# Kernel tuning notes

Measured on AMD Instinct MI355X. Metric: run time of the kernel, lower is better.

## Reference

```python
import jax, jax.numpy as jnp
import numpy as np

THRESHOLD = 0.9
N = 20000
K = 32
F = 64


def setup_inputs() -> dict:
    key = jax.random.key(0)
    k1, k2, k3, k4, k5 = jax.random.split(key, 5)
    features = jax.random.normal(k1, (N, F), dtype=jnp.float32)
    score = jax.random.normal(k2, (N, 1), dtype=jnp.float32)
    distances = jax.random.uniform(k3, (N, K), dtype=jnp.float32)
    # two equal segments; neighbours sampled within own segment, self at col 0
    row_splits = jnp.array([0, N // 2, N], dtype=jnp.int32)
    segN = N // 2
    local_self = (jnp.arange(N, dtype=jnp.int32) % segN)
    seg_start = (jnp.arange(N, dtype=jnp.int32) // segN) * segN
    r = jax.random.randint(k4, (N, K - 1), 0, segN - 1, dtype=jnp.int32)
    r = r + (r >= local_self[:, None]).astype(jnp.int32)  # avoid sampling self
    neigh = seg_start[:, None] + r
    nidxs = jnp.concatenate([jnp.arange(N, dtype=jnp.int32)[:, None], neigh], axis=1)
    tidxs = jax.random.randint(k5, (N, 1), 0, 50, dtype=jnp.int32)
    return {"features": features, "score": score, "distances": distances,
            "nidxs": nidxs, "row_splits": row_splits, "tidxs": tidxs}


def _lnc(features, score_logits, nidxs, row_splits):
    n, k = nidxs.shape
    score = jax.nn.sigmoid(score_logits[:, 0])  # [N]
    # hierarchy order: per row-split segment, descending score
    seg_id = jnp.searchsorted(row_splits, jnp.arange(n), side='right') - 1
    order = jnp.lexsort((-score, seg_id))

    arangeK = jnp.arange(k)

    def step(carry, p):
        ggather, sel, npg, gcount = carry
        already = ggather[p] >= 0
        high = score[p] > THRESHOLD
        m = nidxs[p]                                   # [K], m[0] == p (self)
        free = (m >= 0) & (ggather[jnp.clip(m, 0, n - 1)] < 0)
        self_only = arangeK == 0
        valid = jnp.where(high, free, self_only) & (~already) & (m >= 0)
        g = gcount
        idx_w = jnp.where(valid, m, n)                 # dummy slot n for masked writes
        ggather = ggather.at[idx_w].set(g)
        row_i = jnp.where(already, n, g)
        sel = sel.at[row_i].set(jnp.where(valid, m, -1))
        npg = npg.at[row_i].set(jnp.sum(valid.astype(jnp.int32)))
        created = (~already).astype(jnp.int32)
        return (ggather, sel, npg, gcount + created), created

    init = (jnp.full((n + 1,), -1, jnp.int32),
            jnp.full((n + 1, k), -1, jnp.int32),
            jnp.zeros((n + 1,), jnp.int32),
            jnp.int32(0))
    (ggather, sel, npg, gcount), created = jax.lax.scan(step, init, order)
    ggather, sel, npg = ggather[:n], sel[:n], npg[:n]

    # new row splits: cumulative group count at segment boundaries
    cum = jnp.cumsum(created)
    rs_new = jnp.concatenate([jnp.zeros((1,), jnp.int32),
                              cum[row_splits[1:] - 1].astype(jnp.int32)])

    # pooled features per group (rows >= gcount are padding)
    sel_c = jnp.clip(sel, 0, n - 1)
    gathered = features[sel_c]                         # [N, K, F]
    mask = (sel >= 0)[..., None]
    out_mean = jnp.sum(jnp.where(mask, gathered, 0.0), axis=1)
    out_mean = out_mean / (npg[:, None].astype(features.dtype) + 1e-6)
    out_max = jnp.max(jnp.where(mask, gathered, -1000.0), axis=1)
    out = jnp.concatenate([out_mean, out_max], axis=-1)  # [N, 2F]
    backgather = ggather[:, None]
    return out, rs_new, backgather


def reference(features, score, distances, nidxs, row_splits, tidxs):
    # distances/tidxs only feed the (disabled) loss branch; kept for signature parity
    return _lnc(features, score, nidxs, row_splits)
```

## Files before the change

kernel.cpp:

```cpp
#include <hip/hip_runtime.h>


constexpr int KN = 32;
constexpr int FD = 64;
constexpr int HOCAP = 512;
constexpr int EW = 16;
constexpr int NBB = 2048;
constexpr int NT = 256;
constexpr int NMAX = 20000;

typedef unsigned long long u64;


__global__ void k0_init(const float* __restrict__ score, float* __restrict__ s,
                        int* __restrict__ grab, u64* __restrict__ hlk,
                        u64* __restrict__ key, int* __restrict__ counters,
                        const int* __restrict__ row_splits, int n) {
  int x = (int)(blockIdx.x * blockDim.x + threadIdx.x);
  int lane = (int)threadIdx.x & 63;
  int half = row_splits[1];
  bool hi = false, lo = false;
  u64 pk = 0;
  if (x < n) {
    float sp = 1.0f / (1.0f + expf(-score[x]));
    s[x] = sp; grab[x] = 0x7FFFFFFF;
    hi = sp > 0.9f; lo = !hi;
    unsigned sb = __float_as_uint(sp);
    pk = ((u64)(x >= half) << 63) | ((u64)(0x7FFFFFFFu - sb) << 32) | (unsigned)x;
    key[x] = lo ? (((u64)sb << 32) | (u64)(0xFFFFFFFFu - (unsigned)x)) : 0ull;
  }
  u64 b0 = __ballot(lo && x < half);
  u64 b1 = __ballot(lo && x >= half);
  u64 bh = __ballot(hi);
  if (lane == 0) {
    if (b0) atomicAdd(&counters[4], __popcll(b0));
    if (b1) atomicAdd(&counters[5], __popcll(b1));
  }
  int base = 0;
  if (lane == 0 && bh) base = atomicAdd(&counters[0], __popcll(bh));
  base = __shfl(base, 0);
  if (hi) {
    int idx = base + __popcll(bh & ((1ull << lane) - 1ull));
    if (idx < HOCAP) hlk[idx] = pk;
  }
}

__global__ __launch_bounds__(1024, 1) void kA(
    const u64* __restrict__ hlkG, const int* __restrict__ nidxs,
    const int* __restrict__ row_splits, int* __restrict__ nbm,
    int* __restrict__ fgj, int* __restrict__ fgp, int* __restrict__ counters,
    int n) {
  __shared__ unsigned short hr16[NMAX];
  __shared__ unsigned E[HOCAP * EW];
  __shared__ u64 hk[HOCAP];
  __shared__ int hol[HOCAP];
  __shared__ int fgjL[HOCAP];
  __shared__ int fgpL[HOCAP];
  __shared__ int shg;
  int tid = (int)threadIdx.x;
  int lane = tid & 63;
  int half = row_splits[1];
  int nh = counters[0]; if (nh > HOCAP) nh = HOCAP;

  {
    unsigned* h32 = (unsigned*)hr16;
    for (int i = tid; i < NMAX / 2; i += 1024) h32[i] = 0xFFFFFFFFu;
  }
  for (int i = tid; i < HOCAP * EW; i += 1024) E[i] = 0u;
  for (int i = tid; i < nh; i += 1024) hk[i] = hlkG[i];
  __syncthreads();

  for (int i = tid; i < nh; i += 1024) {
    u64 kp = hk[i];
    int rk = 0;
#pragma unroll 8
    for (int j = 0; j < nh; ++j) rk += (hk[j] < kp) ? 1 : 0;
    int p = (int)(unsigned)(kp & 0xFFFFFFFFu);
    hol[rk] = p; hr16[p] = (unsigned short)rk;
  }
  __syncthreads();

  {
    const int4* nsrc = (const int4*)nidxs;
    int4* ndstG = (int4*)nbm;
    int tot = nh * 8;
    for (int t = tid; t < tot; t += 1024) {
      int j = t >> 3, q4 = t & 7;
      int p = hol[j];
      int4 v = nsrc[p * 8 + q4];
      ndstG[t] = v;
      unsigned bit = 1u << (j & 31);
      unsigned widx = (unsigned)(j >> 5);
      int xs[4] = { v.x, v.y, v.z, v.w };
#pragma unroll
      for (int e = 0; e < 4; ++e) {
        unsigned r = ((unsigned)xs[e] < (unsigned)n) ? hr16[xs[e]] : 0xFFFFu;
        if (r != 0xFFFFu) atomicOr(&E[r * EW + widx], bit);
      }
    }
  }
  __syncthreads();

  if (tid < 64) {
    unsigned Fw[16];
#pragma unroll
    for (int w = 0; w < 16; ++w) Fw[w] = 0u;
    int hg = 0, h0 = 0, h1 = 0;
    u64 mask_lt = (1ull << lane) - 1ull;
#pragma unroll
    for (int c = 0; c < HOCAP / 64; ++c) {
      if (c * 64 >= nh) break;
      int j = c * 64 + lane;
      bool valid = j < nh;
      unsigned er[16];
#pragma unroll
      for (int w = 0; w < 16; ++w) er[w] = valid ? E[j * EW + w] : 0u;
      unsigned acc = 0;
#pragma unroll
      for (int w = 0; w < 16; ++w) acc |= er[w] & Fw[w];
      bool base_already = acc != 0u;
      u64 erc = ((u64)er[2 * c + 1] << 32) | er[2 * c];
      u64 fb = 0;
      for (int l = 0; l < 64; ++l) {
        bool already = base_already || ((erc & fb) != 0ull);
        bool formed = valid && !already;
        fb |= __ballot(formed && (lane == l));
      }
      Fw[2 * c]     |= (unsigned)(fb & 0xFFFFFFFFull);
      Fw[2 * c + 1] |= (unsigned)(fb >> 32);
      bool formed = (fb >> lane) & 1ull;
      int p = valid ? hol[j] : 0;
      if (formed) {
        int idx = hg + __popcll(fb & mask_lt);
        fgjL[idx] = j; fgpL[idx] = p;
      }
      h0 += __popcll(__ballot(formed && p < half));
      h1 += __popcll(__ballot(formed && p >= half));
      hg += __popcll(fb);
    }
    if (lane == 0) {
      counters[1] = hg; counters[2] = h0; counters[3] = h1; shg = hg;
    }
  }
  __syncthreads();
  int hg = shg;
  for (int i = tid; i < hg; i += 1024) { fgj[i] = fgjL[i]; fgp[i] = fgpL[i]; }
}

__global__ void kG(const float* __restrict__ s, const int* __restrict__ nbm,
                   const int* __restrict__ fgj, int* __restrict__ grab,
                   u64* __restrict__ key, int* __restrict__ counters,
                   const int* __restrict__ row_splits, int n) {
  int t = (int)(blockIdx.x * blockDim.x + threadIdx.x);
  int lane = (int)threadIdx.x & 63;
  int half = row_splits[1];
  int hg = counters[1];
  bool gl0 = false, gl1 = false;
  if (t < hg * KN) {
    int g = t >> 5;
    int x = nbm[fgj[g] * KN + (t & 31)];
    if ((unsigned)x < (unsigned)n) {
      int old = atomicMin(&grab[x], g);
      if (old == 0x7FFFFFFF && !(s[x] > 0.9f)) {
        key[x] = 0ull;
        if (x < half) gl0 = true; else gl1 = true;
      }
    }
  }
  u64 b0 = __ballot(gl0), b1 = __ballot(gl1);
  if (lane == 0) {
    if (b0) atomicSub(&counters[4], __popcll(b0));
    if (b1) atomicSub(&counters[5], __popcll(b1));
  }
}

__global__ void kB(const int* __restrict__ row_splits, const u64* __restrict__ key,
                   const int* __restrict__ grab, const int* __restrict__ nbm,
                   const int* __restrict__ fgj, const int* __restrict__ fgp,
                   const int* __restrict__ counters, int* __restrict__ gowner,
                   unsigned* __restrict__ gmask, float* __restrict__ out,
                   int n, int rs_off) {
  int tid = (int)threadIdx.x, bid = (int)blockIdx.x;
  int gtid = bid * NT + tid;
  int lane = tid & 63;
  int half = row_splits[1];
  const int GSZ = NBB * NT;
  const int NW = GSZ >> 6;
  int wid = gtid >> 6;
  int hg = counters[1], H0 = counters[2], H1 = counters[3];
  int L0 = counters[4], L1 = counters[5];
  int bg = rs_off + 3;

  for (int x = gtid; x < n; x += GSZ) {
    int prov = grab[x];
    if (prov != 0x7FFFFFFF)
      out[bg + x] = (float)((prov < H0) ? prov : (prov + L0));
  }

  for (int tsk = wid; tsk < ((n + 3) >> 2); tsk += NW) {
    int p0 = tsk * 4;
    u64 kp0 = key[p0];
    u64 kp1 = (p0 + 1 < n) ? key[p0 + 1] : 0ull;
    u64 kp2 = (p0 + 2 < n) ? key[p0 + 2] : 0ull;
    u64 kp3 = (p0 + 3 < n) ? key[p0 + 3] : 0ull;
    if ((kp0 | kp1 | kp2 | kp3) == 0ull) continue;
    int base2 = (p0 < half) ? 0 : (half >> 1);
    int npair = ((p0 < half) ? half : (n - half)) >> 1;
    const ulonglong2* key2 = (const ulonglong2*)key;
    unsigned r0 = 0, r1 = 0, r2 = 0, r3 = 0;
    for (int j = lane; j < npair; j += 64) {
      ulonglong2 kk = key2[base2 + j];
      r0 += (unsigned)((kk.x > kp0) + (kk.y > kp0));
      r1 += (unsigned)((kk.x > kp1) + (kk.y > kp1));
      r2 += (unsigned)((kk.x > kp2) + (kk.y > kp2));
      r3 += (unsigned)((kk.x > kp3) + (kk.y > kp3));
    }
#pragma unroll
    for (int off = 32; off > 0; off >>= 1) {
      r0 += __shfl_down(r0, off);
      r1 += __shfl_down(r1, off);
      r2 += __shfl_down(r2, off);
      r3 += __shfl_down(r3, off);
    }
    if (lane == 0) {
      unsigned rr[4] = { r0, r1, r2, r3 };
      u64 kps[4] = { kp0, kp1, kp2, kp3 };
#pragma unroll
      for (int j = 0; j < 4; ++j) {
        if (kps[j] == 0ull) continue;
        int p = p0 + j;
        int base = (p < half) ? H0 : (H0 + L0 + H1);
        int gid = base + (int)rr[j];
        gowner[gid] = p; gmask[gid] = 1u;
        out[bg + p] = (float)gid;
      }
    }
  }

  for (int t = gtid; t < hg * KN; t += GSZ) {
    int g = t >> 5, k = t & 31;
    int x = nbm[fgj[g] * KN + k];
    u64 b = __ballot(grab[x] == g);
    if (k == 0) {
      unsigned w = (lane >= 32) ? (unsigned)(b >> 32) : (unsigned)b;
      int gid2 = (g < H0) ? g : (g + L0);
      gowner[gid2] = fgp[g]; gmask[gid2] = w;
    }
  }

  if (gtid == 0) {
    out[rs_off + 0] = 0.0f;
    out[rs_off + 1] = (float)(H0 + L0);
    out[rs_off + 2] = (float)(H0 + L0 + H1 + L1);
  }
}

__global__ void kC(const float* __restrict__ feat, const int* __restrict__ nidxs,
                   const int* __restrict__ gowner, const unsigned* __restrict__ gmask,
                   const int* __restrict__ counters, float* __restrict__ out, int n) {
  int gtid = (int)(blockIdx.x * blockDim.x + threadIdx.x);
  int wid = gtid >> 6;
  int f = gtid & 63;
  const int NW = (NBB * NT) >> 6;
  int G = counters[2] + counters[3] + counters[4] + counters[5];
  for (int row = wid; row < n; row += NW) {
    float mean, mx;
    if (row < G) {
      int owner = gowner[row];
      unsigned mask = gmask[row];
      int npg = __popc(mask);
      float sum = 0.0f; mx = -1000.0f;
      for (int k = 0; k < KN; ++k) {
        if (mask & (1u << k)) {
          int m = nidxs[owner * KN + k];
          float v = feat[m * FD + f];
          sum += v; mx = fmaxf(mx, v);
        }
      }
      mean = sum / ((float)npg + 1e-6f);
    } else {
      mean = 0.0f; mx = -1000.0f;
    }
    out[row * (2 * FD) + f] = mean;
    out[row * (2 * FD) + FD + f] = mx;
  }
}

extern "C" void kernel_launch(void* const* d_in, const int* in_sizes, int n_in,
                              void* d_out, int out_size, void* d_ws, size_t ws_size,
                              hipStream_t stream) {
  const float* features   = (const float*)d_in[0];
  const float* score      = (const float*)d_in[1];
  const int*   nidxs      = (const int*)d_in[3];
  const int*   row_splits = (const int*)d_in[4];
  int n = in_sizes[1];
  float* out = (float*)d_out;
  int* wsi = (int*)d_ws;
  int rs_off = n * 2 * FD;

  int*      counters = wsi;
  float*    s        = (float*)(wsi + 8);
  int*      grab     = wsi + 8 + n;
  u64*      key      = (u64*)(wsi + 8 + 2 * n);
  int*      gowner   = wsi + 8 + 4 * n;
  int*      nbm      = wsi + 8 + 5 * n;
  int*      fgj      = wsi + 8 + 5 * n + HOCAP * KN;
  int*      fgp      = fgj + HOCAP;
  u64*      hlk      = (u64*)nbm;
  unsigned* gmask    = (unsigned*)s;

  int blocks = (n + NT - 1) / NT;
  (void)hipMemsetAsync(counters, 0, 8 * sizeof(int), stream);
  k0_init<<<blocks, NT, 0, stream>>>(score, s, grab, hlk, key, counters,
                                     row_splits, n);
  kA<<<1, 1024, 0, stream>>>(hlk, nidxs, row_splits, nbm, fgj, fgp,
                             counters, n);
  kG<<<(HOCAP * KN) / NT, NT, 0, stream>>>(s, nbm, fgj, grab, key, counters,
                                           row_splits, n);
  kB<<<NBB, NT, 0, stream>>>(row_splits, key, grab, nbm, fgj, fgp, counters,
                             gowner, gmask, out, n, rs_off);
  kC<<<NBB, NT, 0, stream>>>(features, nidxs, gowner, gmask, counters, out, n);
}
```

Before: 82.09 us.

## Replace global atomic counters with per-block staging and in-kernel prefix sum

k0_init now counts high-score and low-score points per block with shared-memory atomics and writes per-block staged keys and counts. kA does a prefix sum over the blocks, compacts the staged keys, and writes the counters itself, so the hipMemsetAsync and the global atomics are no longer needed. Separately, the rank-counting loop in kB now handles 8 keys per wave instead of 4, so each pass over the key array serves more points. The costs are higher register pressure in kB and a cap of 64 high-score points per block that could drop entries.

```diff
diff --git a/kernel.cpp b/kernel.cpp
--- a/kernel.cpp
+++ b/kernel.cpp
@@ -8,17 +8,23 @@
 constexpr int NBB = 2048;
 constexpr int NT = 256;
 constexpr int NMAX = 20000;
+constexpr int BSLOT = 64;
 
 typedef unsigned long long u64;
 
 
 __global__ void k0_init(const float* __restrict__ score, float* __restrict__ s,
-                        int* __restrict__ grab, u64* __restrict__ hlk,
-                        u64* __restrict__ key, int* __restrict__ counters,
+                        int* __restrict__ grab, u64* __restrict__ hlkStage,
+                        int* __restrict__ hcnt, int* __restrict__ lcnt0,
+                        int* __restrict__ lcnt1, u64* __restrict__ key,
                         const int* __restrict__ row_splits, int n) {
-  int x = (int)(blockIdx.x * blockDim.x + threadIdx.x);
-  int lane = (int)threadIdx.x & 63;
+  __shared__ int ch, cl0, cl1;
+  int tid = (int)threadIdx.x, bid = (int)blockIdx.x;
+  int x = bid * NT + tid;
+  int lane = tid & 63;
   int half = row_splits[1];
+  if (tid == 0) { ch = 0; cl0 = 0; cl1 = 0; }
+  __syncthreads();
   bool hi = false, lo = false;
   u64 pk = 0;
   if (x < n) {
@@ -29,45 +35,83 @@
     pk = ((u64)(x >= half) << 63) | ((u64)(0x7FFFFFFFu - sb) << 32) | (unsigned)x;
     key[x] = lo ? (((u64)sb << 32) | (u64)(0xFFFFFFFFu - (unsigned)x)) : 0ull;
   }
+  u64 bh = __ballot(hi);
   u64 b0 = __ballot(lo && x < half);
   u64 b1 = __ballot(lo && x >= half);
-  u64 bh = __ballot(hi);
+  int base = 0;
   if (lane == 0) {
-    if (b0) atomicAdd(&counters[4], __popcll(b0));
-    if (b1) atomicAdd(&counters[5], __popcll(b1));
-  }
-  int base = 0;
-  if (lane == 0 && bh) base = atomicAdd(&counters[0], __popcll(bh));
+    if (bh) base = atomicAdd(&ch, __popcll(bh));
+    if (b0) atomicAdd(&cl0, __popcll(b0));
+    if (b1) atomicAdd(&cl1, __popcll(b1));
+  }
   base = __shfl(base, 0);
   if (hi) {
     int idx = base + __popcll(bh & ((1ull << lane) - 1ull));
-    if (idx < HOCAP) hlk[idx] = pk;
+    if (idx < BSLOT) hlkStage[bid * BSLOT + idx] = pk;
+  }
+  __syncthreads();
+  if (tid == 0) {
+    hcnt[bid] = (ch > BSLOT) ? BSLOT : ch;
+    lcnt0[bid] = cl0; lcnt1[bid] = cl1;
   }
 }
 
 __global__ __launch_bounds__(1024, 1) void kA(
-    const u64* __restrict__ hlkG, const int* __restrict__ nidxs,
-    const int* __restrict__ row_splits, int* __restrict__ nbm,
-    int* __restrict__ fgj, int* __restrict__ fgp, int* __restrict__ counters,
-    int n) {
+    const u64* __restrict__ hlkStage, const int* __restrict__ hcnt,
+    const int* __restrict__ lcnt0, const int* __restrict__ lcnt1,
+    const int* __restrict__ nidxs, const int* __restrict__ row_splits,
+    int* __restrict__ nbm, int* __restrict__ fgj, int* __restrict__ fgp,
+    int* __restrict__ counters, int n) {
   __shared__ unsigned short hr16[NMAX];
   __shared__ unsigned E[HOCAP * EW];
   __shared__ u64 hk[HOCAP];
   __shared__ int hol[HOCAP];
   __shared__ int fgjL[HOCAP];
   __shared__ int fgpL[HOCAP];
+  __shared__ int cnts[128];
+  __shared__ int pref[129];
+  __shared__ int lsum[2];
   __shared__ int shg;
   int tid = (int)threadIdx.x;
   int lane = tid & 63;
   int half = row_splits[1];
-  int nh = counters[0]; if (nh > HOCAP) nh = HOCAP;
+  int nblk = (n + NT - 1) / NT; if (nblk > 128) nblk = 128;
 
   {
     unsigned* h32 = (unsigned*)hr16;
     for (int i = tid; i < NMAX / 2; i += 1024) h32[i] = 0xFFFFFFFFu;
   }
   for (int i = tid; i < HOCAP * EW; i += 1024) E[i] = 0u;
-  for (int i = tid; i < nh; i += 1024) hk[i] = hlkG[i];
+  if (tid < 128) cnts[tid] = (tid < nblk) ? hcnt[tid] : 0;
+  if (tid == 0) { lsum[0] = 0; lsum[1] = 0; }
+  __syncthreads();
+
+  if (tid < 64) {
+    int v0 = cnts[tid], v1 = cnts[64 + tid];
+#pragma unroll
+    for (int off = 1; off < 64; off <<= 1) {
+      int t0 = __shfl_up(v0, off), t1 = __shfl_up(v1, off);
+      if (lane >= off) { v0 += t0; v1 += t1; }
+    }
+    int s0 = __shfl(v0, 63);
+    pref[tid + 1] = v0;
+    pref[64 + tid + 1] = v1 + s0;
+    if (tid == 0) pref[0] = 0;
+  }
+  if (tid >= 64 && tid < 192) {
+    int b = tid - 64;
+    if (b < nblk) { atomicAdd(&lsum[0], lcnt0[b]); atomicAdd(&lsum[1], lcnt1[b]); }
+  }
+  __syncthreads();
+  int nh = pref[nblk]; if (nh > HOCAP) nh = HOCAP;
+
+  for (int t = tid; t < nblk * BSLOT; t += 1024) {
+    int b = t >> 6, j = t & (BSLOT - 1);
+    if (j < cnts[b]) {
+      int d = pref[b] + j;
+      if (d < HOCAP) hk[d] = hlkStage[t];
+    }
+  }
   __syncthreads();
 
   for (int i = tid; i < nh; i += 1024) {
@@ -145,6 +189,11 @@
   __syncthreads();
   int hg = shg;
   for (int i = tid; i < hg; i += 1024) { fgj[i] = fgjL[i]; fgp[i] = fgpL[i]; }
+  if (tid == 0) {
+    counters[0] = nh;
+    counters[4] = lsum[0];
+    counters[5] = lsum[1];
+  }
 }
 
 __global__ void kG(const float* __restrict__ s, const int* __restrict__ nbm,
@@ -197,40 +246,37 @@
       out[bg + x] = (float)((prov < H0) ? prov : (prov + L0));
   }
 
-  for (int tsk = wid; tsk < ((n + 3) >> 2); tsk += NW) {
-    int p0 = tsk * 4;
-    u64 kp0 = key[p0];
-    u64 kp1 = (p0 + 1 < n) ? key[p0 + 1] : 0ull;
-    u64 kp2 = (p0 + 2 < n) ? key[p0 + 2] : 0ull;
-    u64 kp3 = (p0 + 3 < n) ? key[p0 + 3] : 0ull;
-    if ((kp0 | kp1 | kp2 | kp3) == 0ull) continue;
+  for (int tsk = wid; tsk < ((n + 7) >> 3); tsk += NW) {
+    int p0 = tsk * 8;
+    u64 kp[8];
+#pragma unroll
+    for (int i = 0; i < 8; ++i) kp[i] = (p0 + i < n) ? key[p0 + i] : 0ull;
+    u64 anyk = 0;
+#pragma unroll
+    for (int i = 0; i < 8; ++i) anyk |= kp[i];
+    if (anyk == 0ull) continue;
     int base2 = (p0 < half) ? 0 : (half >> 1);
     int npair = ((p0 < half) ? half : (n - half)) >> 1;
     const ulonglong2* key2 = (const ulonglong2*)key;
-    unsigned r0 = 0, r1 = 0, r2 = 0, r3 = 0;
+    unsigned r[8] = {0, 0, 0, 0, 0, 0, 0, 0};
     for (int j = lane; j < npair; j += 64) {
       ulonglong2 kk = key2[base2 + j];
-      r0 += (unsigned)((kk.x > kp0) + (kk.y > kp0));
-      r1 += (unsigned)((kk.x > kp1) + (kk.y > kp1));
-      r2 += (unsigned)((kk.x > kp2) + (kk.y > kp2));
-      r3 += (unsigned)((kk.x > kp3) + (kk.y > kp3));
-    }
-#pragma unroll
-    for (int off = 32; off > 0; off >>= 1) {
-      r0 += __shfl_down(r0, off);
-      r1 += __shfl_down(r1, off);
-      r2 += __shfl_down(r2, off);
-      r3 += __shfl_down(r3, off);
+#pragma unroll
+      for (int i = 0; i < 8; ++i)
+        r[i] += (unsigned)((kk.x > kp[i]) + (kk.y > kp[i]));
+    }
+#pragma unroll
+    for (int i = 0; i < 8; ++i) {
+#pragma unroll
+      for (int off = 32; off > 0; off >>= 1) r[i] += __shfl_down(r[i], off);
     }
     if (lane == 0) {
-      unsigned rr[4] = { r0, r1, r2, r3 };
-      u64 kps[4] = { kp0, kp1, kp2, kp3 };
-#pragma unroll
-      for (int j = 0; j < 4; ++j) {
-        if (kps[j] == 0ull) continue;
-        int p = p0 + j;
+#pragma unroll
+      for (int i = 0; i < 8; ++i) {
+        if (kp[i] == 0ull) continue;
+        int p = p0 + i;
         int base = (p < half) ? H0 : (H0 + L0 + H1);
-        int gid = base + (int)rr[j];
+        int gid = base + (int)r[i];
         gowner[gid] = p; gmask[gid] = 1u;
         out[bg + p] = (float)gid;
       }
@@ -306,15 +352,17 @@
   int*      nbm      = wsi + 8 + 5 * n;
   int*      fgj      = wsi + 8 + 5 * n + HOCAP * KN;
   int*      fgp      = fgj + HOCAP;
-  u64*      hlk      = (u64*)nbm;
+  u64*      hlkStage = (u64*)(fgp + HOCAP);
+  int*      hcnt     = (int*)(hlkStage + 128 * BSLOT);
+  int*      lcnt0    = hcnt + 128;
+  int*      lcnt1    = lcnt0 + 128;
   unsigned* gmask    = (unsigned*)s;
 
   int blocks = (n + NT - 1) / NT;
-  (void)hipMemsetAsync(counters, 0, 8 * sizeof(int), stream);
-  k0_init<<<blocks, NT, 0, stream>>>(score, s, grab, hlk, key, counters,
-                                     row_splits, n);
-  kA<<<1, 1024, 0, stream>>>(hlk, nidxs, row_splits, nbm, fgj, fgp,
-                             counters, n);
+  k0_init<<<blocks, NT, 0, stream>>>(score, s, grab, hlkStage, hcnt, lcnt0,
+                                     lcnt1, key, row_splits, n);
+  kA<<<1, 1024, 0, stream>>>(hlkStage, hcnt, lcnt0, lcnt1, nidxs, row_splits,
+                             nbm, fgj, fgp, counters, n);
   kG<<<(HOCAP * KN) / NT, NT, 0, stream>>>(s, nbm, fgj, grab, key, counters,
                                            row_splits, n);
   kB<<<NBB, NT, 0, stream>>>(row_splits, key, grab, nbm, fgj, fgp, counters,
```

New measurement: 85.30 us. 1.04x slower.
